# Optimization experiments

Hardware: AMD Instinct MI355X
Metric: run time of the kernel (lower is better)

Reference implementation:

```python
import jax, jax.numpy as jnp
import numpy as np
from jax import lax

SEQ_LEN, PRED_LEN = 336, 96
BATCH, D, H, GATES = 1024, 64, 64, 4 * 64  # input_dim must equal hidden_dim (see forward feedback)


def setup_inputs() -> dict:
    key = jax.random.key(0)
    ks = jax.random.split(key, 11)
    s = 1.0 / np.sqrt(H)  # PyTorch-style uniform-ish scale, via scaled normals
    return {
        "x": jax.random.normal(ks[0], (BATCH, SEQ_LEN, D), dtype=jnp.float32),
        "W_ih0": jax.random.normal(ks[1], (GATES, D), dtype=jnp.float32) * s,
        "W_hh0": jax.random.normal(ks[2], (GATES, H), dtype=jnp.float32) * s,
        "b_ih0": jax.random.normal(ks[3], (GATES,), dtype=jnp.float32) * s,
        "b_hh0": jax.random.normal(ks[4], (GATES,), dtype=jnp.float32) * s,
        "W_ih1": jax.random.normal(ks[5], (GATES, H), dtype=jnp.float32) * s,
        "W_hh1": jax.random.normal(ks[6], (GATES, H), dtype=jnp.float32) * s,
        "b_ih1": jax.random.normal(ks[7], (GATES,), dtype=jnp.float32) * s,
        "b_hh1": jax.random.normal(ks[8], (GATES,), dtype=jnp.float32) * s,
        "W_fc": jax.random.normal(ks[9], (D, H), dtype=jnp.float32) * s,
        "b_fc": jax.random.normal(ks[10], (D,), dtype=jnp.float32) * s,
    }


def _gates(pre):
    # PyTorch gate order: input, forget, cell(g), output
    i, f, g, o = jnp.split(pre, 4, axis=-1)
    return jax.nn.sigmoid(i), jax.nn.sigmoid(f), jnp.tanh(g), jax.nn.sigmoid(o)


def _lstm_layer_seq(x, W_ih, W_hh, b_ih, b_hh):
    """Run one LSTM layer over full sequence, zero initial state. x: [B,T,I] -> [B,T,H]."""
    B = x.shape[0]
    x_pre = jnp.einsum('bti,gi->btg', x, W_ih) + b_ih + b_hh  # precompute input projections
    h0 = jnp.zeros((B, W_hh.shape[1]), x.dtype)
    c0 = jnp.zeros_like(h0)

    def step(carry, xt_pre):
        h, c = carry
        i, f, g, o = _gates(xt_pre + h @ W_hh.T)
        c = f * c + i * g
        h = o * jnp.tanh(c)
        return (h, c), h

    _, hs = lax.scan(step, (h0, c0), jnp.swapaxes(x_pre, 0, 1))  # [T,B,H]
    return jnp.swapaxes(hs, 0, 1)


def _lstm_single_step_zero_state(xt, layers):
    """One LSTM time step with ZERO initial state (matches passing hidden=None each step).
    With h=c=0: c = i*g, h = o*tanh(c). xt: [B,D] -> [B,H]."""
    inp = xt
    for (W_ih, W_hh, b_ih, b_hh) in layers:
        i, f, g, o = _gates(inp @ W_ih.T + b_ih + b_hh)  # h=0 so W_hh term vanishes
        c = i * g
        inp = o * jnp.tanh(c)
        del W_hh, f
    return inp


def reference(x, W_ih0, W_hh0, b_ih0, b_hh0, W_ih1, W_hh1, b_ih1, b_hh1, W_fc, b_fc):
    # --- encode: 2-layer LSTM over the input sequence ---
    h1 = _lstm_layer_seq(x, W_ih0, W_hh0, b_ih0, b_hh0)
    h2 = _lstm_layer_seq(h1, W_ih1, W_hh1, b_ih1, b_hh1)
    current = h2[:, -1, :]  # [B,H]; fed back as rnn input (requires H == input_dim)

    layers = ((W_ih0, W_hh0, b_ih0, b_hh0), (W_ih1, W_hh1, b_ih1, b_hh1))

    def dec(carry, _):
        h = _lstm_single_step_zero_state(carry, layers)
        pred = h @ W_fc.T + b_fc
        return pred, pred

    _, preds = lax.scan(dec, current, None, length=PRED_LEN)  # [P,B,D]
    return jnp.swapaxes(preds, 0, 1)  # [B,P,D]
```

## Files before the change

### kernel.cpp

```cpp
#include <hip/hip_runtime.h>

#define NB    1024
#define TSEQ  336
#define DIM   64
#define GATES 256
#define PRED  96


__device__ __forceinline__ float sigm(float v)  { return 1.0f / (1.0f + __expf(-v)); }
__device__ __forceinline__ float tanh_(float v) { return 1.0f - 2.0f / (__expf(2.0f * v) + 1.0f); }

__device__ __forceinline__ void fma4v(float& acc, const float4 xv, const float4 w) {
    acc = fmaf(xv.x, w.x, acc); acc = fmaf(xv.y, w.y, acc);
    acc = fmaf(xv.z, w.z, acc); acc = fmaf(xv.w, w.w, acc);
}

extern "C" __global__ void __launch_bounds__(512, 4)
gemm_pre(const float* __restrict__ in,
         const float* __restrict__ W,
         const float* __restrict__ ba, const float* __restrict__ bb,
         float* __restrict__ pre,
         int tcount)
{
    __shared__ __align__(16) float xt[2][512];
    __shared__ __align__(16) float pp[2 * 2048];
    const int tid = threadIdx.x;
    const int row = blockIdx.x;
    const int g   = tid & 255;
    const int kh  = tid >> 8;

    float4 w[8];
#pragma unroll
    for (int k4 = 0; k4 < 8; ++k4)
        w[k4] = *reinterpret_cast<const float4*>(W + g * DIM + kh * 32 + k4 * 4);
    const float bs = ba[g] + bb[g];

    const float* rin  = in  + (size_t)row * (TSEQ * DIM);
    float*       rout = pre + (size_t)row * tcount * GATES;
    const int ntile = tcount >> 3;

    xt[0][tid] = rin[tid];
    __syncthreads();
    for (int tile = 0; tile < ntile; ++tile) {
        const int cur = tile & 1;
        float pa[8];
#pragma unroll
        for (int t8 = 0; t8 < 8; ++t8) {
            const float* xb = &xt[cur][t8 * 64 + kh * 32];
            float a = 0.f;
#pragma unroll
            for (int k4 = 0; k4 < 8; ++k4)
                fma4v(a, *reinterpret_cast<const float4*>(xb + k4 * 4), w[k4]);
            pa[t8] = a;
        }
#pragma unroll
        for (int t8 = 0; t8 < 8; ++t8)
            pp[kh * 2048 + t8 * 256 + g] = pa[t8];
        if (tile + 1 < ntile)
            xt[cur ^ 1][tid] = rin[(tile + 1) * 512 + tid];
        __syncthreads();
        const int tb = tile * 8;
#pragma unroll
        for (int q = 0; q < 4; ++q) {
            const int t8 = q * 2 + kh;
            rout[(size_t)(tb + t8) * GATES + g] =
                pp[t8 * 256 + g] + pp[2048 + t8 * 256 + g] + bs;
        }
        __syncthreads();
    }
}

extern "C" __global__ void __launch_bounds__(512, 4)
lstm_recur(const float* __restrict__ pre, int tcount, int t0,
           const float* __restrict__ Whh,
           float* __restrict__ hseq,
           float* __restrict__ hstate, float* __restrict__ cstate,
           int zero_init)
{
    __shared__ __align__(16) float Hs[128];
    __shared__ __align__(16) float Ps[1024];
    const int tid = threadIdx.x;
    const int r0  = blockIdx.x * 2;
    const int g   = tid & 255;
    const int kh  = tid >> 8;
    const int rr  = (tid >> 6) & 1;
    const int jj  = tid & 63;

    float4 w[8];
#pragma unroll
    for (int k4 = 0; k4 < 8; ++k4)
        w[k4] = *reinterpret_cast<const float4*>(Whh + g * DIM + kh * 32 + k4 * 4);

    const size_t prow = (size_t)tcount * GATES;
    float c = 0.f;
    float pvA0 = 0.f, pvA1 = 0.f, pvA2 = 0.f, pvA3 = 0.f;
    float pvB0 = 0.f, pvB1 = 0.f, pvB2 = 0.f, pvB3 = 0.f;
    if (tid < 128) {
        if (zero_init) Hs[tid] = 0.f;
        else { Hs[tid] = hstate[(r0 + rr) * DIM + jj]; c = cstate[(r0 + rr) * DIM + jj]; }
        const float* p0 = pre + (size_t)(r0 + rr) * prow + jj;
        pvA0 = p0[0]; pvA1 = p0[64]; pvA2 = p0[128]; pvA3 = p0[192];
        const float* p1 = p0 + GATES;
        pvB0 = p1[0]; pvB1 = p1[64]; pvB2 = p1[128]; pvB3 = p1[192];
    }
    __syncthreads();

    float hlast = 0.f;
    for (int t = 0; t < tcount; ++t) {
        float a0 = 0.f, a1 = 0.f;
        const float* hb0 = Hs + kh * 32;
        const float* hb1 = Hs + 64 + kh * 32;
#pragma unroll
        for (int k4 = 0; k4 < 8; ++k4) {
            fma4v(a0, *reinterpret_cast<const float4*>(hb0 + k4 * 4), w[k4]);
            fma4v(a1, *reinterpret_cast<const float4*>(hb1 + k4 * 4), w[k4]);
        }
        Ps[kh * 512 + g]       = a0;
        Ps[kh * 512 + 256 + g] = a1;
        __syncthreads();

        if (tid < 128) {
            float xi = pvA0, xf = pvA1, xg = pvA2, xo = pvA3;
            pvA0 = pvB0; pvA1 = pvB1; pvA2 = pvB2; pvA3 = pvB3;
            if (t + 2 < tcount) {
                const float* pp = pre + (size_t)(r0 + rr) * prow + (size_t)(t + 2) * GATES + jj;
                pvB0 = pp[0]; pvB1 = pp[64]; pvB2 = pp[128]; pvB3 = pp[192];
            }
            const float* q0 = Ps + rr * 256 + jj;
            const float* q1 = Ps + 512 + rr * 256 + jj;
            xi += q0[0]   + q1[0];
            xf += q0[64]  + q1[64];
            xg += q0[128] + q1[128];
            xo += q0[192] + q1[192];
            const float ig = sigm(xi), fg = sigm(xf), gg = tanh_(xg), og = sigm(xo);
            c = fmaf(fg, c, ig * gg);
            const float h = og * tanh_(c);
            hlast = h;
            Hs[tid] = h;
            if (hseq) hseq[(size_t)(r0 + rr) * (TSEQ * DIM) + (size_t)(t0 + t) * DIM + jj] = h;
        }
        __syncthreads();
    }
    if (tid < 128) {
        hstate[(r0 + rr) * DIM + jj] = hlast;
        cstate[(r0 + rr) * DIM + jj] = c;
    }
}

#define DWFC 0
#define DP0  4096
#define DP1  4608
#define DH0  5120
#define DH1  5248
#define DDB  5376
#define DBS0 5504
#define DBS1 5760
#define DBFC 6016
#define DSMF 6080

extern "C" __global__ void __launch_bounds__(512, 2)
lstm_dec(const float* __restrict__ Wih0, const float* __restrict__ Wih1,
         const float* __restrict__ Wfc,
         const float* __restrict__ bih0, const float* __restrict__ bhh0,
         const float* __restrict__ bih1, const float* __restrict__ bhh1,
         const float* __restrict__ bfc,
         const float* __restrict__ h1last, float* __restrict__ out)
{
    __shared__ __align__(16) float sm[DSMF];
    const int tid = threadIdx.x;
    const int r0  = blockIdx.x * 2;
    const int rr  = (tid >> 6) & 1;
    const int jj  = tid & 63;
    const int dsub = tid >> 8;
    const int g0d  = tid & 255;

    if (tid < 256) {
        sm[DBS0 + tid] = bih0[tid] + bhh0[tid];
        sm[DBS1 + tid] = bih1[tid] + bhh1[tid];
    }
    if (tid < 64) sm[DBFC + tid] = bfc[tid];
    for (int idx = tid; idx < DIM * DIM; idx += 512) {
        const int j = idx >> 6, k = idx & 63;
        sm[DWFC + (k >> 2) * 256 + (k & 3) * 64 + j] = Wfc[idx];
    }
    if (tid < 128) sm[DDB + tid] = h1last[(r0 + rr) * DIM + jj];

    const float* Wsrc = dsub ? Wih1 : Wih0;
    float4 wd[16];
#pragma unroll
    for (int k4 = 0; k4 < 16; ++k4)
        wd[k4] = *reinterpret_cast<const float4*>(Wsrc + g0d * DIM + k4 * 4);
    __syncthreads();
    const float bfc_j = sm[DBFC + jj];

    for (int p = 0; p < PRED; ++p) {
        if (dsub == 0) {
            float a0 = 0.f, a1 = 0.f;
#pragma unroll
            for (int k4 = 0; k4 < 16; ++k4) {
                fma4v(a0, *reinterpret_cast<const float4*>(sm + DDB + k4 * 4),      wd[k4]);
                fma4v(a1, *reinterpret_cast<const float4*>(sm + DDB + 64 + k4 * 4), wd[k4]);
            }
            sm[DP0 + g0d] = a0; sm[DP0 + 256 + g0d] = a1;
        }
        __syncthreads();
        if (tid < 128) {
            const float* q = sm + DP0 + rr * 256;
            const float pi = sm[DBS0 + jj]        + q[jj];
            const float pg = sm[DBS0 + 128 + jj]  + q[128 + jj];
            const float po = sm[DBS0 + 192 + jj]  + q[192 + jj];
            const float ig = sigm(pi), gg = tanh_(pg), og = sigm(po);
            sm[DH0 + tid] = og * tanh_(ig * gg);
        }
        __syncthreads();
        if (dsub == 1) {
            float a0 = 0.f, a1 = 0.f;
#pragma unroll
            for (int k4 = 0; k4 < 16; ++k4) {
                fma4v(a0, *reinterpret_cast<const float4*>(sm + DH0 + k4 * 4),      wd[k4]);
                fma4v(a1, *reinterpret_cast<const float4*>(sm + DH0 + 64 + k4 * 4), wd[k4]);
            }
            sm[DP1 + g0d] = a0; sm[DP1 + 256 + g0d] = a1;
        }
        __syncthreads();
        if (tid < 128) {
            const float* q = sm + DP1 + rr * 256;
            const float pi = sm[DBS1 + jj]        + q[jj];
            const float pg = sm[DBS1 + 128 + jj]  + q[128 + jj];
            const float po = sm[DBS1 + 192 + jj]  + q[192 + jj];
            const float ig = sigm(pi), gg = tanh_(pg), og = sigm(po);
            sm[DH1 + tid] = og * tanh_(ig * gg);
            float acc = bfc_j;
            const float4* hp = reinterpret_cast<const float4*>(sm + DH1 + rr * 64);
#pragma unroll
            for (int k4 = 0; k4 < 16; ++k4) {
                const float4 hv = hp[k4];
                const float* wp = sm + DWFC + k4 * 256;
                acc = fmaf(hv.x, wp[jj],       acc);
                acc = fmaf(hv.y, wp[64 + jj],  acc);
                acc = fmaf(hv.z, wp[128 + jj], acc);
                acc = fmaf(hv.w, wp[192 + jj], acc);
            }
            out[(size_t)(r0 + rr) * PRED * DIM + p * DIM + jj] = acc;
            sm[DDB + tid] = acc;
        }
        __syncthreads();
    }
}

#define BP0O   0
#define BP1O   4096
#define BWFCO  8192
#define BH0O   12288
#define BH1O   12544
#define BDBO   12800
#define BBS0O  13056
#define BBS1O  13312
#define BBFCO  13568
#define BSMF   13632
#define BSMEM_BYTES (BSMF * 4)

extern "C" __global__ void __launch_bounds__(512, 2)
rnn_fused_base(const float* __restrict__ x,
          const float* __restrict__ Wih0, const float* __restrict__ Whh0,
          const float* __restrict__ bih0, const float* __restrict__ bhh0,
          const float* __restrict__ Wih1, const float* __restrict__ Whh1,
          const float* __restrict__ bih1, const float* __restrict__ bhh1,
          const float* __restrict__ Wfc,  const float* __restrict__ bfc,
          float* __restrict__ out)
{
    extern __shared__ float sm[];
    const int tid = threadIdx.x;
    const int bid = blockIdx.x;
    const int grp = tid >> 7;
    const int m   = grp & 1;
    const int kh  = grp >> 1;
    const int gp  = tid & 127;
    const int g0  = gp, g1 = gp + 128;
    const int rr  = (tid & 255) >> 6;
    const int jj  = tid & 63;

    if (tid < GATES) {
        sm[BBS0O + tid] = bih0[tid] + bhh0[tid];
        sm[BBS1O + tid] = bih1[tid] + bhh1[tid];
    }
    if (tid < DIM) sm[BBFCO + tid] = bfc[tid];
    if (tid < 256) { sm[BH0O + tid] = 0.0f; sm[BH1O + tid] = 0.0f; }
    for (int idx = tid; idx < DIM * DIM; idx += 512) {
        const int j = idx >> 6, k = idx & 63;
        sm[BWFCO + (k >> 2) * 256 + (k & 3) * 64 + j] = Wfc[idx];
    }

    const float* Wsrc0 = m ? Whh0 : Wih0;
    const float* Wsrc1 = m ? Whh1 : Wih1;
    float4 w0a[8], w0b[8], w1a[8], w1b[8];
#pragma unroll
    for (int k4 = 0; k4 < 8; ++k4) {
        w0a[k4] = *reinterpret_cast<const float4*>(Wsrc0 + g0 * DIM + kh * 32 + k4 * 4);
        w0b[k4] = *reinterpret_cast<const float4*>(Wsrc0 + g1 * DIM + kh * 32 + k4 * 4);
        w1a[k4] = *reinterpret_cast<const float4*>(Wsrc1 + g0 * DIM + kh * 32 + k4 * 4);
        w1b[k4] = *reinterpret_cast<const float4*>(Wsrc1 + g1 * DIM + kh * 32 + k4 * 4);
    }
    __syncthreads();

    const int row0 = bid * 4;
    const float* xr0 = x + (size_t)(row0 + 0) * TSEQ * DIM + kh * 32;
    const float* xr1 = x + (size_t)(row0 + 1) * TSEQ * DIM + kh * 32;
    const float* xr2 = x + (size_t)(row0 + 2) * TSEQ * DIM + kh * 32;
    const float* xr3 = x + (size_t)(row0 + 3) * TSEQ * DIM + kh * 32;

    const int pb = grp * 1024;
    float c_state = 0.0f;

    for (int s = 0; s < TSEQ; ++s) {
        if (s != 0 && tid >= 256) {
            float pi = sm[BBS1O + jj],       pf = sm[BBS1O + 64 + jj];
            float pg = sm[BBS1O + 128 + jj], po = sm[BBS1O + 192 + jj];
#pragma unroll
            for (int cp = 0; cp < 4; ++cp) {
                const float* p = sm + BP1O + cp * 1024 + rr * 256;
                pi += p[jj]; pf += p[64 + jj]; pg += p[128 + jj]; po += p[192 + jj];
            }
            const float ig = sigm(pi), fg = sigm(pf), gg = tanh_(pg), og = sigm(po);
            c_state = fmaf(fg, c_state, ig * gg);
            sm[BH1O + (tid & 255)] = og * tanh_(c_state);
        }
        {
            float acc[8];
#pragma unroll
            for (int i = 0; i < 8; ++i) acc[i] = 0.0f;
            if (m == 0) {
                const int so = s * DIM;
#pragma unroll
                for (int k4 = 0; k4 < 8; ++k4) {
                    const float4 v0 = *reinterpret_cast<const float4*>(xr0 + so + k4 * 4);
                    const float4 v1 = *reinterpret_cast<const float4*>(xr1 + so + k4 * 4);
                    const float4 v2 = *reinterpret_cast<const float4*>(xr2 + so + k4 * 4);
                    const float4 v3 = *reinterpret_cast<const float4*>(xr3 + so + k4 * 4);
                    fma4v(acc[0], v0, w0a[k4]); fma4v(acc[1], v0, w0b[k4]);
                    fma4v(acc[2], v1, w0a[k4]); fma4v(acc[3], v1, w0b[k4]);
                    fma4v(acc[4], v2, w0a[k4]); fma4v(acc[5], v2, w0b[k4]);
                    fma4v(acc[6], v3, w0a[k4]); fma4v(acc[7], v3, w0b[k4]);
                }
            } else {
#pragma unroll
                for (int k4 = 0; k4 < 8; ++k4) {
                    const float4 v0 = *reinterpret_cast<const float4*>(sm + BH0O + 0 * 64 + kh * 32 + k4 * 4);
                    const float4 v1 = *reinterpret_cast<const float4*>(sm + BH0O + 1 * 64 + kh * 32 + k4 * 4);
                    const float4 v2 = *reinterpret_cast<const float4*>(sm + BH0O + 2 * 64 + kh * 32 + k4 * 4);
                    const float4 v3 = *reinterpret_cast<const float4*>(sm + BH0O + 3 * 64 + kh * 32 + k4 * 4);
                    fma4v(acc[0], v0, w0a[k4]); fma4v(acc[1], v0, w0b[k4]);
                    fma4v(acc[2], v1, w0a[k4]); fma4v(acc[3], v1, w0b[k4]);
                    fma4v(acc[4], v2, w0a[k4]); fma4v(acc[5], v2, w0b[k4]);
                    fma4v(acc[6], v3, w0a[k4]); fma4v(acc[7], v3, w0b[k4]);
                }
            }
            sm[BP0O + pb + 0 * 256 + g0] = acc[0]; sm[BP0O + pb + 0 * 256 + g1] = acc[1];
            sm[BP0O + pb + 1 * 256 + g0] = acc[2]; sm[BP0O + pb + 1 * 256 + g1] = acc[3];
            sm[BP0O + pb + 2 * 256 + g0] = acc[4]; sm[BP0O + pb + 2 * 256 + g1] = acc[5];
            sm[BP0O + pb + 3 * 256 + g0] = acc[6]; sm[BP0O + pb + 3 * 256 + g1] = acc[7];
        }
        __syncthreads();

        if (tid < 256) {
            float pi = sm[BBS0O + jj],       pf = sm[BBS0O + 64 + jj];
            float pg = sm[BBS0O + 128 + jj], po = sm[BBS0O + 192 + jj];
#pragma unroll
            for (int cp = 0; cp < 4; ++cp) {
                const float* p = sm + BP0O + cp * 1024 + rr * 256;
                pi += p[jj]; pf += p[64 + jj]; pg += p[128 + jj]; po += p[192 + jj];
            }
            const float ig = sigm(pi), fg = sigm(pf), gg = tanh_(pg), og = sigm(po);
            c_state = fmaf(fg, c_state, ig * gg);
            sm[BH0O + tid] = og * tanh_(c_state);
        }
        __syncthreads();

        {
            const int ib = m ? BH1O : BH0O;
            float acc[8];
#pragma unroll
            for (int i = 0; i < 8; ++i) acc[i] = 0.0f;
#pragma unroll
            for (int k4 = 0; k4 < 8; ++k4) {
                const float4 v0 = *reinterpret_cast<const float4*>(sm + ib + 0 * 64 + kh * 32 + k4 * 4);
                const float4 v1 = *reinterpret_cast<const float4*>(sm + ib + 1 * 64 + kh * 32 + k4 * 4);
                const float4 v2 = *reinterpret_cast<const float4*>(sm + ib + 2 * 64 + kh * 32 + k4 * 4);
                const float4 v3 = *reinterpret_cast<const float4*>(sm + ib + 3 * 64 + kh * 32 + k4 * 4);
                fma4v(acc[0], v0, w1a[k4]); fma4v(acc[1], v0, w1b[k4]);
                fma4v(acc[2], v1, w1a[k4]); fma4v(acc[3], v1, w1b[k4]);
                fma4v(acc[4], v2, w1a[k4]); fma4v(acc[5], v2, w1b[k4]);
                fma4v(acc[6], v3, w1a[k4]); fma4v(acc[7], v3, w1b[k4]);
            }
            sm[BP1O + pb + 0 * 256 + g0] = acc[0]; sm[BP1O + pb + 0 * 256 + g1] = acc[1];
            sm[BP1O + pb + 1 * 256 + g0] = acc[2]; sm[BP1O + pb + 1 * 256 + g1] = acc[3];
            sm[BP1O + pb + 2 * 256 + g0] = acc[4]; sm[BP1O + pb + 2 * 256 + g1] = acc[5];
            sm[BP1O + pb + 3 * 256 + g0] = acc[6]; sm[BP1O + pb + 3 * 256 + g1] = acc[7];
        }
        __syncthreads();
    }

    if (tid >= 256) {
        float pi = sm[BBS1O + jj],       pf = sm[BBS1O + 64 + jj];
        float pg = sm[BBS1O + 128 + jj], po = sm[BBS1O + 192 + jj];
#pragma unroll
        for (int cp = 0; cp < 4; ++cp) {
            const float* p = sm + BP1O + cp * 1024 + rr * 256;
            pi += p[jj]; pf += p[64 + jj]; pg += p[128 + jj]; po += p[192 + jj];
        }
        const float ig = sigm(pi), fg = sigm(pf), gg = tanh_(pg), og = sigm(po);
        c_state = fmaf(fg, c_state, ig * gg);
        sm[BDBO + (tid & 255)] = og * tanh_(c_state);
    }
    __syncthreads();

    const float bfc_j = sm[BBFCO + jj];

    for (int p = 0; p < PRED; ++p) {
        if (m == 0) {
            float acc[8];
#pragma unroll
            for (int i = 0; i < 8; ++i) acc[i] = 0.0f;
#pragma unroll
            for (int k4 = 0; k4 < 8; ++k4) {
                const float4 v0 = *reinterpret_cast<const float4*>(sm + BDBO + 0 * 64 + kh * 32 + k4 * 4);
                const float4 v1 = *reinterpret_cast<const float4*>(sm + BDBO + 1 * 64 + kh * 32 + k4 * 4);
                const float4 v2 = *reinterpret_cast<const float4*>(sm + BDBO + 2 * 64 + kh * 32 + k4 * 4);
                const float4 v3 = *reinterpret_cast<const float4*>(sm + BDBO + 3 * 64 + kh * 32 + k4 * 4);
                fma4v(acc[0], v0, w0a[k4]); fma4v(acc[1], v0, w0b[k4]);
                fma4v(acc[2], v1, w0a[k4]); fma4v(acc[3], v1, w0b[k4]);
                fma4v(acc[4], v2, w0a[k4]); fma4v(acc[5], v2, w0b[k4]);
                fma4v(acc[6], v3, w0a[k4]); fma4v(acc[7], v3, w0b[k4]);
            }
            sm[BP0O + pb + 0 * 256 + g0] = acc[0]; sm[BP0O + pb + 0 * 256 + g1] = acc[1];
            sm[BP0O + pb + 1 * 256 + g0] = acc[2]; sm[BP0O + pb + 1 * 256 + g1] = acc[3];
            sm[BP0O + pb + 2 * 256 + g0] = acc[4]; sm[BP0O + pb + 2 * 256 + g1] = acc[5];
            sm[BP0O + pb + 3 * 256 + g0] = acc[6]; sm[BP0O + pb + 3 * 256 + g1] = acc[7];
        }
        __syncthreads();
        if (tid < 256) {
            float pi = sm[BBS0O + jj], pg = sm[BBS0O + 128 + jj], po = sm[BBS0O + 192 + jj];
            {
                const float* pA = sm + BP0O + 0 * 1024 + rr * 256;
                const float* pB = sm + BP0O + 2 * 1024 + rr * 256;
                pi += pA[jj] + pB[jj];
                pg += pA[128 + jj] + pB[128 + jj];
                po += pA[192 + jj] + pB[192 + jj];
            }
            const float ig = sigm(pi), gg = tanh_(pg), og = sigm(po);
            sm[BH0O + tid] = og * tanh_(ig * gg);
        }
        __syncthreads();

        if (m == 0) {
            float acc[8];
#pragma unroll
            for (int i = 0; i < 8; ++i) acc[i] = 0.0f;
#pragma unroll
            for (int k4 = 0; k4 < 8; ++k4) {
                const float4 v0 = *reinterpret_cast<const float4*>(sm + BH0O + 0 * 64 + kh * 32 + k4 * 4);
                const float4 v1 = *reinterpret_cast<const float4*>(sm + BH0O + 1 * 64 + kh * 32 + k4 * 4);
                const float4 v2 = *reinterpret_cast<const float4*>(sm + BH0O + 2 * 64 + kh * 32 + k4 * 4);
                const float4 v3 = *reinterpret_cast<const float4*>(sm + BH0O + 3 * 64 + kh * 32 + k4 * 4);
                fma4v(acc[0], v0, w1a[k4]); fma4v(acc[1], v0, w1b[k4]);
                fma4v(acc[2], v1, w1a[k4]); fma4v(acc[3], v1, w1b[k4]);
                fma4v(acc[4], v2, w1a[k4]); fma4v(acc[5], v2, w1b[k4]);
                fma4v(acc[6], v3, w1a[k4]); fma4v(acc[7], v3, w1b[k4]);
            }
            sm[BP1O + pb + 0 * 256 + g0] = acc[0]; sm[BP1O + pb + 0 * 256 + g1] = acc[1];
            sm[BP1O + pb + 1 * 256 + g0] = acc[2]; sm[BP1O + pb + 1 * 256 + g1] = acc[3];
            sm[BP1O + pb + 2 * 256 + g0] = acc[4]; sm[BP1O + pb + 2 * 256 + g1] = acc[5];
            sm[BP1O + pb + 3 * 256 + g0] = acc[6]; sm[BP1O + pb + 3 * 256 + g1] = acc[7];
        }
        __syncthreads();
        if (tid >= 256) {
            float pi = sm[BBS1O + jj], pg = sm[BBS1O + 128 + jj], po = sm[BBS1O + 192 + jj];
            {
                const float* pA = sm + BP1O + 0 * 1024 + rr * 256;
                const float* pB = sm + BP1O + 2 * 1024 + rr * 256;
                pi += pA[jj] + pB[jj];
                pg += pA[128 + jj] + pB[128 + jj];
                po += pA[192 + jj] + pB[192 + jj];
            }
            const float ig = sigm(pi), gg = tanh_(pg), og = sigm(po);
            sm[BH1O + (tid & 255)] = og * tanh_(ig * gg);
        }
        __syncthreads();

        if (tid < 256) {
            float acc = bfc_j;
            const float4* hp = reinterpret_cast<const float4*>(sm + BH1O + rr * 64);
#pragma unroll
            for (int k4 = 0; k4 < 16; ++k4) {
                const float4 hv = hp[k4];
                const float* wp = sm + BWFCO + k4 * 256;
                acc = fmaf(hv.x, wp[jj],       acc);
                acc = fmaf(hv.y, wp[64 + jj],  acc);
                acc = fmaf(hv.z, wp[128 + jj], acc);
                acc = fmaf(hv.w, wp[192 + jj], acc);
            }
            out[(size_t)(row0 + rr) * PRED * DIM + p * DIM + jj] = acc;
            sm[BDBO + tid] = acc;
        }
        __syncthreads();
    }
}

extern "C" void kernel_launch(void* const* d_in, const int* in_sizes, int n_in,
                              void* d_out, int out_size, void* d_ws, size_t ws_size,
                              hipStream_t stream) {
    const float* x    = (const float*)d_in[0];
    const float* Wih0 = (const float*)d_in[1];
    const float* Whh0 = (const float*)d_in[2];
    const float* bih0 = (const float*)d_in[3];
    const float* bhh0 = (const float*)d_in[4];
    const float* Wih1 = (const float*)d_in[5];
    const float* Whh1 = (const float*)d_in[6];
    const float* bih1 = (const float*)d_in[7];
    const float* bhh1 = (const float*)d_in[8];
    const float* Wfc  = (const float*)d_in[9];
    const float* bfc  = (const float*)d_in[10];
    float* out = (float*)d_out;

    const size_t base_fl = 4 * (size_t)NB * DIM + (size_t)NB * TSEQ * DIM;
    int tc = 0;
    if (d_ws) {
        const int cands[3] = {336, 168, 112};
        for (int i = 0; i < 3; ++i) {
            const size_t need = (base_fl + (size_t)NB * cands[i] * GATES) * 4;
            if (ws_size >= need) { tc = cands[i]; break; }
        }
    }
    if (tc == 0) {
        hipLaunchKernelGGL(rnn_fused_base, dim3(NB / 4), dim3(512), BSMEM_BYTES, stream,
                           x, Wih0, Whh0, bih0, bhh0, Wih1, Whh1, bih1, bhh1, Wfc, bfc, out);
        return;
    }

    float* wsf   = (float*)d_ws;
    float* st0h  = wsf;
    float* st0c  = wsf + (size_t)NB * DIM;
    float* st1h  = wsf + 2 * (size_t)NB * DIM;
    float* st1c  = wsf + 3 * (size_t)NB * DIM;
    float* h0seq = wsf + 4 * (size_t)NB * DIM;
    float* pre   = wsf + base_fl;

    const int nch = TSEQ / tc;
    for (int i = 0; i < nch; ++i) {
        const int t0 = i * tc;
        hipLaunchKernelGGL(gemm_pre, dim3(NB), dim3(512), 0, stream,
                           x + (size_t)t0 * DIM, Wih0, bih0, bhh0, pre, tc);
        hipLaunchKernelGGL(lstm_recur, dim3(NB / 2), dim3(512), 0, stream,
                           pre, tc, t0, Whh0, h0seq, st0h, st0c, (int)(i == 0));
        hipLaunchKernelGGL(gemm_pre, dim3(NB), dim3(512), 0, stream,
                           h0seq + (size_t)t0 * DIM, Wih1, bih1, bhh1, pre, tc);
        hipLaunchKernelGGL(lstm_recur, dim3(NB / 2), dim3(512), 0, stream,
                           pre, tc, t0, Whh1, (float*)nullptr, st1h, st1c, (int)(i == 0));
    }
    hipLaunchKernelGGL(lstm_dec, dim3(NB / 2), dim3(512), 0, stream,
                       Wih0, Wih1, Wfc, bih0, bhh0, bih1, bhh1, bfc, st1h, out);
}
```

Measured before the change: 1.428 ms.

## Restructure LSTM recurrence to full-K dot per thread with shuffle gate exchange

Result: slower. 1.835 ms (+28.5%).

```diff
diff --git a/kernel.cpp b/kernel.cpp
--- a/kernel.cpp
+++ b/kernel.cpp
@@ -28,6 +28,7 @@
     const int row = blockIdx.x;
     const int g   = tid & 255;
     const int kh  = tid >> 8;
+    const int gperm = (g & 63) * 4 + (g >> 6);
 
     float4 w[8];
 #pragma unroll
@@ -63,7 +64,7 @@
 #pragma unroll
         for (int q = 0; q < 4; ++q) {
             const int t8 = q * 2 + kh;
-            rout[(size_t)(tb + t8) * GATES + g] =
+            rout[(size_t)(tb + t8) * GATES + gperm] =
                 pp[t8 * 256 + g] + pp[2048 + t8 * 256 + g] + bs;
         }
         __syncthreads();
@@ -77,73 +78,70 @@
            float* __restrict__ hstate, float* __restrict__ cstate,
            int zero_init)
 {
-    __shared__ __align__(16) float Hs[128];
-    __shared__ __align__(16) float Ps[1024];
-    const int tid = threadIdx.x;
-    const int r0  = blockIdx.x * 2;
-    const int g   = tid & 255;
-    const int kh  = tid >> 8;
-    const int rr  = (tid >> 6) & 1;
-    const int jj  = tid & 63;
-
-    float4 w[8];
-#pragma unroll
-    for (int k4 = 0; k4 < 8; ++k4)
-        w[k4] = *reinterpret_cast<const float4*>(Whh + g * DIM + kh * 32 + k4 * 4);
-
-    const size_t prow = (size_t)tcount * GATES;
-    float c = 0.f;
-    float pvA0 = 0.f, pvA1 = 0.f, pvA2 = 0.f, pvA3 = 0.f;
-    float pvB0 = 0.f, pvB1 = 0.f, pvB2 = 0.f, pvB3 = 0.f;
-    if (tid < 128) {
-        if (zero_init) Hs[tid] = 0.f;
-        else { Hs[tid] = hstate[(r0 + rr) * DIM + jj]; c = cstate[(r0 + rr) * DIM + jj]; }
-        const float* p0 = pre + (size_t)(r0 + rr) * prow + jj;
-        pvA0 = p0[0]; pvA1 = p0[64]; pvA2 = p0[128]; pvA3 = p0[192];
-        const float* p1 = p0 + GATES;
-        pvB0 = p1[0]; pvB1 = p1[64]; pvB2 = p1[128]; pvB3 = p1[192];
-    }
+    __shared__ __align__(16) float Hs[2][128];
+    const int tid  = threadIdx.x;
+    const int r0   = blockIdx.x * 2;
+    const int row  = tid >> 8;
+    const int lidx = tid & 255;
+    const int j    = lidx >> 2;
+    const int gate = lidx & 3;
+    const int grow = gate * 64 + j;
+
+    float4 w[16];
+#pragma unroll
+    for (int k4 = 0; k4 < 16; ++k4)
+        w[k4] = *reinterpret_cast<const float4*>(Whh + grow * DIM + k4 * 4);
+
+    float c;
+    if (zero_init) {
+        c = 0.f;
+        if (gate == 0) Hs[0][row * 64 + j] = 0.f;
+    } else {
+        c = cstate[(r0 + row) * DIM + j];
+        if (gate == 0) Hs[0][row * 64 + j] = hstate[(r0 + row) * DIM + j];
+    }
+    const float* prow = pre + (size_t)(r0 + row) * tcount * GATES + lidx;
+    float pvA = prow[0];
+    float pvB = prow[GATES];
     __syncthreads();
 
-    float hlast = 0.f;
+    int cur = 0;
+    float h = 0.f;
     for (int t = 0; t < tcount; ++t) {
-        float a0 = 0.f, a1 = 0.f;
-        const float* hb0 = Hs + kh * 32;
-        const float* hb1 = Hs + 64 + kh * 32;
-#pragma unroll
-        for (int k4 = 0; k4 < 8; ++k4) {
-            fma4v(a0, *reinterpret_cast<const float4*>(hb0 + k4 * 4), w[k4]);
-            fma4v(a1, *reinterpret_cast<const float4*>(hb1 + k4 * 4), w[k4]);
-        }
-        Ps[kh * 512 + g]       = a0;
-        Ps[kh * 512 + 256 + g] = a1;
-        __syncthreads();
-
-        if (tid < 128) {
-            float xi = pvA0, xf = pvA1, xg = pvA2, xo = pvA3;
-            pvA0 = pvB0; pvA1 = pvB1; pvA2 = pvB2; pvA3 = pvB3;
-            if (t + 2 < tcount) {
-                const float* pp = pre + (size_t)(r0 + rr) * prow + (size_t)(t + 2) * GATES + jj;
-                pvB0 = pp[0]; pvB1 = pp[64]; pvB2 = pp[128]; pvB3 = pp[192];
-            }
-            const float* q0 = Ps + rr * 256 + jj;
-            const float* q1 = Ps + 512 + rr * 256 + jj;
-            xi += q0[0]   + q1[0];
-            xf += q0[64]  + q1[64];
-            xg += q0[128] + q1[128];
-            xo += q0[192] + q1[192];
-            const float ig = sigm(xi), fg = sigm(xf), gg = tanh_(xg), og = sigm(xo);
-            c = fmaf(fg, c, ig * gg);
-            const float h = og * tanh_(c);
-            hlast = h;
-            Hs[tid] = h;
-            if (hseq) hseq[(size_t)(r0 + rr) * (TSEQ * DIM) + (size_t)(t0 + t) * DIM + jj] = h;
-        }
-        __syncthreads();
-    }
-    if (tid < 128) {
-        hstate[(r0 + rr) * DIM + jj] = hlast;
-        cstate[(r0 + rr) * DIM + jj] = c;
+        float xa = pvA, xb = 0.f;
+        pvA = pvB;
+        if (t + 2 < tcount) pvB = prow[(size_t)(t + 2) * GATES];
+        const float* hb = Hs[cur] + row * 64;
+#pragma unroll
+        for (int k4 = 0; k4 < 16; k4 += 2) {
+            fma4v(xa, *reinterpret_cast<const float4*>(hb + k4 * 4),       w[k4]);
+            fma4v(xb, *reinterpret_cast<const float4*>(hb + (k4 + 1) * 4), w[k4 + 1]);
+        }
+        const float x = xa + xb;
+        const float v1 = __shfl_xor(x, 1, 64);
+        const float v2 = __shfl_xor(x, 2, 64);
+        const float v3 = __shfl_xor(v1, 2, 64);
+        const float vi = (gate == 0) ? x : (gate == 1) ? v1 : (gate == 2) ? v2 : v3;
+        const int mf = gate ^ 1;
+        const float vf = (mf == 0) ? x : (mf == 1) ? v1 : (mf == 2) ? v2 : v3;
+        const int mg = gate ^ 2;
+        const float vg = (mg == 0) ? x : (mg == 1) ? v1 : (mg == 2) ? v2 : v3;
+        const int mo = gate ^ 3;
+        const float vo = (mo == 0) ? x : (mo == 1) ? v1 : (mo == 2) ? v2 : v3;
+
+        const float ig = sigm(vi), fg = sigm(vf), gg = tanh_(vg), og = sigm(vo);
+        c = fmaf(fg, c, ig * gg);
+        h = og * tanh_(c);
+        if (gate == 0) {
+            Hs[cur ^ 1][row * 64 + j] = h;
+            if (hseq) hseq[(size_t)(r0 + row) * (TSEQ * DIM) + (size_t)(t0 + t) * DIM + j] = h;
+        }
+        __syncthreads();
+        cur ^= 1;
+    }
+    if (gate == 0) {
+        hstate[(r0 + row) * DIM + j] = h;
+        cstate[(r0 + row) * DIM + j] = c;
     }
 }
 
```

## Replace shared-memory tiled input projection with shuffle-based per-step reduction

Applied to the files above, without the earlier changes.

Result: slower. 3.421 ms (+139.6%).

```diff
diff --git a/kernel.cpp b/kernel.cpp
--- a/kernel.cpp
+++ b/kernel.cpp
@@ -22,12 +22,10 @@
          float* __restrict__ pre,
          int tcount)
 {
-    __shared__ __align__(16) float xt[2][512];
-    __shared__ __align__(16) float pp[2 * 2048];
     const int tid = threadIdx.x;
     const int row = blockIdx.x;
-    const int g   = tid & 255;
-    const int kh  = tid >> 8;
+    const int g   = tid >> 1;
+    const int kh  = tid & 1;
 
     float4 w[8];
 #pragma unroll
@@ -35,38 +33,18 @@
         w[k4] = *reinterpret_cast<const float4*>(W + g * DIM + kh * 32 + k4 * 4);
     const float bs = ba[g] + bb[g];
 
-    const float* rin  = in  + (size_t)row * (TSEQ * DIM);
+    const float* rin  = in  + (size_t)row * (TSEQ * DIM) + kh * 32;
     float*       rout = pre + (size_t)row * tcount * GATES;
-    const int ntile = tcount >> 3;
-
-    xt[0][tid] = rin[tid];
-    __syncthreads();
-    for (int tile = 0; tile < ntile; ++tile) {
-        const int cur = tile & 1;
-        float pa[8];
-#pragma unroll
-        for (int t8 = 0; t8 < 8; ++t8) {
-            const float* xb = &xt[cur][t8 * 64 + kh * 32];
-            float a = 0.f;
-#pragma unroll
-            for (int k4 = 0; k4 < 8; ++k4)
-                fma4v(a, *reinterpret_cast<const float4*>(xb + k4 * 4), w[k4]);
-            pa[t8] = a;
-        }
-#pragma unroll
-        for (int t8 = 0; t8 < 8; ++t8)
-            pp[kh * 2048 + t8 * 256 + g] = pa[t8];
-        if (tile + 1 < ntile)
-            xt[cur ^ 1][tid] = rin[(tile + 1) * 512 + tid];
-        __syncthreads();
-        const int tb = tile * 8;
-#pragma unroll
-        for (int q = 0; q < 4; ++q) {
-            const int t8 = q * 2 + kh;
-            rout[(size_t)(tb + t8) * GATES + g] =
-                pp[t8 * 256 + g] + pp[2048 + t8 * 256 + g] + bs;
-        }
-        __syncthreads();
+
+    for (int t = 0; t < tcount; ++t) {
+        const float* xb = rin + t * DIM;
+        float a = 0.f;
+#pragma unroll
+        for (int k4 = 0; k4 < 8; ++k4)
+            fma4v(a, *reinterpret_cast<const float4*>(xb + k4 * 4), w[k4]);
+        const float full = a + __shfl_xor(a, 1, 64);
+        if (kh == 0)
+            rout[(size_t)t * GATES + g] = full + bs;
     }
 }
 
```

## Fuse layer-1 input projection into layer-0 recurrence, drop h0seq round trip

Applied to the files above, without the earlier changes.

Result: slower. 1.817 ms (+27.2%).

```diff
diff --git a/kernel.cpp b/kernel.cpp
--- a/kernel.cpp
+++ b/kernel.cpp
@@ -67,6 +67,102 @@
                 pp[t8 * 256 + g] + pp[2048 + t8 * 256 + g] + bs;
         }
         __syncthreads();
+    }
+}
+
+extern "C" __global__ void __launch_bounds__(512, 2)
+recur_fused(float* __restrict__ pre,
+            const float* __restrict__ Whh0,
+            const float* __restrict__ Wih1,
+            const float* __restrict__ bih1, const float* __restrict__ bhh1,
+            float* __restrict__ hstate, float* __restrict__ cstate)
+{
+    __shared__ __align__(16) float Hs[128];
+    __shared__ __align__(16) float Ps[512];
+    const int tid  = threadIdx.x;
+    const int r0   = blockIdx.x * 2;
+    const int grpB = tid >> 8;
+    const int g    = tid & 255;
+    const int rr   = (tid >> 6) & 1;
+    const int jj   = tid & 63;
+
+    const float* Wsrc = grpB ? Wih1 : Whh0;
+    float4 w[16];
+#pragma unroll
+    for (int k4 = 0; k4 < 16; ++k4)
+        w[k4] = *reinterpret_cast<const float4*>(Wsrc + g * DIM + k4 * 4);
+    const float bs1 = grpB ? (bih1[g] + bhh1[g]) : 0.f;
+
+    const size_t prow = (size_t)TSEQ * GATES;
+    float* preW0 = pre + (size_t)(r0 + 0) * prow;
+    float* preW1 = pre + (size_t)(r0 + 1) * prow;
+
+    float c = 0.f;
+    float pvA0 = 0.f, pvA1 = 0.f, pvA2 = 0.f, pvA3 = 0.f;
+    float pvB0 = 0.f, pvB1 = 0.f, pvB2 = 0.f, pvB3 = 0.f;
+    if (tid < 128) {
+        Hs[tid] = 0.f;
+        const float* p0 = pre + (size_t)(r0 + rr) * prow + jj;
+        pvA0 = p0[0]; pvA1 = p0[64]; pvA2 = p0[128]; pvA3 = p0[192];
+        const float* p1 = p0 + GATES;
+        pvB0 = p1[0]; pvB1 = p1[64]; pvB2 = p1[128]; pvB3 = p1[192];
+    }
+    __syncthreads();
+
+    float hlast = 0.f;
+    for (int t = 0; t < TSEQ; ++t) {
+        if (!grpB) {
+            float a0 = 0.f, a1 = 0.f;
+#pragma unroll
+            for (int k4 = 0; k4 < 16; ++k4) {
+                fma4v(a0, *reinterpret_cast<const float4*>(Hs + k4 * 4),      w[k4]);
+                fma4v(a1, *reinterpret_cast<const float4*>(Hs + 64 + k4 * 4), w[k4]);
+            }
+            Ps[g]       = a0;
+            Ps[256 + g] = a1;
+        } else if (t != 0) {
+            float a0 = bs1, a1 = bs1;
+#pragma unroll
+            for (int k4 = 0; k4 < 16; ++k4) {
+                fma4v(a0, *reinterpret_cast<const float4*>(Hs + k4 * 4),      w[k4]);
+                fma4v(a1, *reinterpret_cast<const float4*>(Hs + 64 + k4 * 4), w[k4]);
+            }
+            preW0[(size_t)(t - 1) * GATES + g] = a0;
+            preW1[(size_t)(t - 1) * GATES + g] = a1;
+        }
+        __syncthreads();
+
+        if (tid < 128) {
+            float xi = pvA0, xf = pvA1, xg = pvA2, xo = pvA3;
+            pvA0 = pvB0; pvA1 = pvB1; pvA2 = pvB2; pvA3 = pvB3;
+            if (t + 2 < TSEQ) {
+                const float* pp = pre + (size_t)(r0 + rr) * prow + (size_t)(t + 2) * GATES + jj;
+                pvB0 = pp[0]; pvB1 = pp[64]; pvB2 = pp[128]; pvB3 = pp[192];
+            }
+            const float* q = Ps + rr * 256 + jj;
+            xi += q[0]; xf += q[64]; xg += q[128]; xo += q[192];
+            const float ig = sigm(xi), fg = sigm(xf), gg = tanh_(xg), og = sigm(xo);
+            c = fmaf(fg, c, ig * gg);
+            const float h = og * tanh_(c);
+            hlast = h;
+            Hs[tid] = h;
+        }
+        __syncthreads();
+    }
+
+    if (grpB) {
+        float a0 = bs1, a1 = bs1;
+#pragma unroll
+        for (int k4 = 0; k4 < 16; ++k4) {
+            fma4v(a0, *reinterpret_cast<const float4*>(Hs + k4 * 4),      w[k4]);
+            fma4v(a1, *reinterpret_cast<const float4*>(Hs + 64 + k4 * 4), w[k4]);
+        }
+        preW0[(size_t)(TSEQ - 1) * GATES + g] = a0;
+        preW1[(size_t)(TSEQ - 1) * GATES + g] = a1;
+    }
+    if (tid < 128) {
+        hstate[(r0 + rr) * DIM + jj] = hlast;
+        cstate[(r0 + rr) * DIM + jj] = c;
     }
 }
 
@@ -522,41 +618,29 @@
     const float* bfc  = (const float*)d_in[10];
     float* out = (float*)d_out;
 
-    const size_t base_fl = 4 * (size_t)NB * DIM + (size_t)NB * TSEQ * DIM;
-    int tc = 0;
-    if (d_ws) {
-        const int cands[3] = {336, 168, 112};
-        for (int i = 0; i < 3; ++i) {
-            const size_t need = (base_fl + (size_t)NB * cands[i] * GATES) * 4;
-            if (ws_size >= need) { tc = cands[i]; break; }
-        }
-    }
-    if (tc == 0) {
+    const size_t state_fl = 4 * (size_t)NB * DIM;
+    const size_t pre_fl   = (size_t)NB * TSEQ * GATES;
+    const size_t need     = (state_fl + pre_fl) * 4;
+
+    if (d_ws == nullptr || ws_size < need) {
         hipLaunchKernelGGL(rnn_fused_base, dim3(NB / 4), dim3(512), BSMEM_BYTES, stream,
                            x, Wih0, Whh0, bih0, bhh0, Wih1, Whh1, bih1, bhh1, Wfc, bfc, out);
         return;
     }
 
-    float* wsf   = (float*)d_ws;
-    float* st0h  = wsf;
-    float* st0c  = wsf + (size_t)NB * DIM;
-    float* st1h  = wsf + 2 * (size_t)NB * DIM;
-    float* st1c  = wsf + 3 * (size_t)NB * DIM;
-    float* h0seq = wsf + 4 * (size_t)NB * DIM;
-    float* pre   = wsf + base_fl;
-
-    const int nch = TSEQ / tc;
-    for (int i = 0; i < nch; ++i) {
-        const int t0 = i * tc;
-        hipLaunchKernelGGL(gemm_pre, dim3(NB), dim3(512), 0, stream,
-                           x + (size_t)t0 * DIM, Wih0, bih0, bhh0, pre, tc);
-        hipLaunchKernelGGL(lstm_recur, dim3(NB / 2), dim3(512), 0, stream,
-                           pre, tc, t0, Whh0, h0seq, st0h, st0c, (int)(i == 0));
-        hipLaunchKernelGGL(gemm_pre, dim3(NB), dim3(512), 0, stream,
-                           h0seq + (size_t)t0 * DIM, Wih1, bih1, bhh1, pre, tc);
-        hipLaunchKernelGGL(lstm_recur, dim3(NB / 2), dim3(512), 0, stream,
-                           pre, tc, t0, Whh1, (float*)nullptr, st1h, st1c, (int)(i == 0));
-    }
+    float* wsf  = (float*)d_ws;
+    float* st0h = wsf;
+    float* st0c = wsf + (size_t)NB * DIM;
+    float* st1h = wsf + 2 * (size_t)NB * DIM;
+    float* st1c = wsf + 3 * (size_t)NB * DIM;
+    float* pre  = wsf + state_fl;
+
+    hipLaunchKernelGGL(gemm_pre, dim3(NB), dim3(512), 0, stream,
+                       x, Wih0, bih0, bhh0, pre, TSEQ);
+    hipLaunchKernelGGL(recur_fused, dim3(NB / 2), dim3(512), 0, stream,
+                       pre, Whh0, Wih1, bih1, bhh1, st0h, st0c);
+    hipLaunchKernelGGL(lstm_recur, dim3(NB / 2), dim3(512), 0, stream,
+                       pre, TSEQ, 0, Whh1, (float*)nullptr, st1h, st1c, 1);
     hipLaunchKernelGGL(lstm_dec, dim3(NB / 2), dim3(512), 0, stream,
                        Wih0, Wih1, Wfc, bih0, bhh0, bih1, bhh1, bfc, st1h, out);
 }
```
